# Performance work log

Measured on AMD Instinct MI355X. Metric: run time of the kernel, lower is better.

## Reference

```python
import jax, jax.numpy as jnp
import numpy as np

E = 8      # number of parts/experts
H = 128    # hidden width
D_IN = 3   # xyz coords
D_OUT = 1  # occupancy


def setup_inputs() -> dict:
    key = jax.random.key(0)
    ks = jax.random.split(key, 9)
    coords = jax.random.normal(ks[0], (1, 65536, D_IN), dtype=jnp.float32)
    s = 0.05
    return {
        "coords": coords,
        "W0": jax.random.normal(ks[1], (E, H, D_IN), dtype=jnp.float32) * s,
        "b0": jax.random.normal(ks[2], (E, H), dtype=jnp.float32) * s,
        "W1": jax.random.normal(ks[3], (E, H, H), dtype=jnp.float32) * s,
        "b1": jax.random.normal(ks[4], (E, H), dtype=jnp.float32) * s,
        "W2": jax.random.normal(ks[5], (E, H, H), dtype=jnp.float32) * s,
        "b2": jax.random.normal(ks[6], (E, H), dtype=jnp.float32) * s,
        "Wo": jax.random.normal(ks[7], (E, D_OUT, H), dtype=jnp.float32) * s,
        "bo": jax.random.normal(ks[8], (E, D_OUT), dtype=jnp.float32) * s,
    }


def reference(coords, W0, b0, W1, b1, W2, b2, Wo, bo):
    # Batched (grouped) MLP over experts: equivalent to vmap(functional_call)
    # over stacked per-part parameters in the torch module.
    # coords: [B, N, 3]; weights: [E, out, in]
    h = jax.nn.relu(jnp.einsum('bnd,ehd->ebnh', coords, W0) + b0[:, None, None, :])
    h = jax.nn.relu(jnp.einsum('ebnh,egh->ebng', h, W1) + b1[:, None, None, :])
    h = jax.nn.relu(jnp.einsum('ebnh,egh->ebng', h, W2) + b2[:, None, None, :])
    expert_out = jnp.einsum('ebnh,eoh->ebno', h, Wo) + bo[:, None, None, :]  # [E,B,N,1]
    max_occ = jnp.max(expert_out, axis=0)  # combine experts via max, [B,N,1]
    return max_occ
```

## Files before the change

### kernel.cpp

```cpp
#include <hip/hip_runtime.h>

#define NE 8
#define HD 128
#define NPTS 65536
#define TM 64

typedef __bf16 bf16x8 __attribute__((ext_vector_type(8)));
typedef float f32x4 __attribute__((ext_vector_type(4)));

__device__ __forceinline__ unsigned int f2bf(float f) {
    unsigned int u = __float_as_uint(f);
    u += 0x7FFFu + ((u >> 16) & 1u);
    return u >> 16;
}
__device__ __forceinline__ float bf2f_lo(unsigned int u) { return __uint_as_float(u << 16); }
__device__ __forceinline__ float bf2f_hi(unsigned int u) { return __uint_as_float(u & 0xFFFF0000u); }

__device__ __forceinline__ unsigned int swz(int row, int byte_in_row) {
    return (unsigned int)((row * 256 + byte_in_row) ^ ((row & 7) << 4));
}

template<int NKB, int BSTR, bool BSWZ>
__device__ __forceinline__ void gemm_gA(const unsigned short* __restrict__ Ag,
                                        const char* Bb, char* Db,
                                        const float* __restrict__ bias,
                                        int w, int lane) {
    const int lr = lane & 15;
    const int lg = lane >> 4;
    const int tc = w * 32;

    f32x4 acc[2][4];
#pragma unroll
    for (int ca = 0; ca < 2; ++ca)
#pragma unroll
        for (int nb = 0; nb < 4; ++nb)
            acc[ca][nb] = (f32x4){0.f, 0.f, 0.f, 0.f};

#pragma unroll
    for (int kb = 0; kb < NKB; ++kb) {
        bf16x8 a[2], b[4];
#pragma unroll
        for (int ca = 0; ca < 2; ++ca) {
            int c = tc + ca * 16 + lr;
            a[ca] = *(const bf16x8*)(Ag + c * (NKB * 32) + kb * 32 + lg * 8);
        }
#pragma unroll
        for (int nb = 0; nb < 4; ++nb) {
            int r = nb * 16 + lr;
            int byte = kb * 64 + lg * 16;
            const char* p = BSWZ ? (Bb + swz(r, byte)) : (Bb + r * BSTR + byte);
            b[nb] = *(const bf16x8*)p;
        }
#pragma unroll
        for (int ca = 0; ca < 2; ++ca)
#pragma unroll
            for (int nb = 0; nb < 4; ++nb)
                acc[ca][nb] = __builtin_amdgcn_mfma_f32_16x16x32_bf16(a[ca], b[nb], acc[ca][nb], 0, 0, 0);
    }

#pragma unroll
    for (int ca = 0; ca < 2; ++ca) {
        int c0 = tc + ca * 16 + lg * 4;
        float4 bs = *(const float4*)(bias + c0);
#pragma unroll
        for (int nb = 0; nb < 4; ++nb) {
            int r = nb * 16 + lr;
            f32x4 v = acc[ca][nb];
            float v0 = fmaxf(v[0] + bs.x, 0.f);
            float v1 = fmaxf(v[1] + bs.y, 0.f);
            float v2 = fmaxf(v[2] + bs.z, 0.f);
            float v3 = fmaxf(v[3] + bs.w, 0.f);
            uint2 p;
            p.x = f2bf(v0) | (f2bf(v1) << 16);
            p.y = f2bf(v2) | (f2bf(v3) << 16);
            *(uint2*)(Db + swz(r, c0 * 2)) = p;
        }
    }
}

__global__ void prep_kernel(const float* __restrict__ W0,
                            const float* __restrict__ W1,
                            const float* __restrict__ W2,
                            unsigned int* __restrict__ W1b,
                            unsigned int* __restrict__ W2b,
                            unsigned int* __restrict__ W0p) {
    int i = blockIdx.x * 256 + threadIdx.x;
    float2 v = *(const float2*)(W1 + 2 * i);
    W1b[i] = f2bf(v.x) | (f2bf(v.y) << 16);
    float2 u = *(const float2*)(W2 + 2 * i);
    W2b[i] = f2bf(u.x) | (f2bf(u.y) << 16);
    if (i < NE * HD * 16) {
        int row = i >> 4;
        int kk = (i & 15) * 2;
        float a = (kk < 3) ? W0[row * 3 + kk] : 0.f;
        float b = (kk + 1 < 3) ? W0[row * 3 + kk + 1] : 0.f;
        W0p[i] = f2bf(a) | (f2bf(b) << 16);
    }
}

__global__ __launch_bounds__(256, 4) void moe_main(
    const float* __restrict__ coords,
    const float* __restrict__ b0, const float* __restrict__ b1,
    const float* __restrict__ b2,
    const float* __restrict__ Wo, const float* __restrict__ bo,
    const unsigned short* __restrict__ W0p,
    const unsigned short* __restrict__ W1b,
    const unsigned short* __restrict__ W2b,
    float* __restrict__ out) {
    __shared__ __align__(16) unsigned short hA[TM * HD];
    __shared__ __align__(16) unsigned short hB[TM * HD];
    __shared__ __align__(16) unsigned short Xp[TM * 40];
    __shared__ __align__(16) float wos[HD];

    const int tid = threadIdx.x;
    const int lane = tid & 63;
    const int w = tid >> 6;
    const int row0 = blockIdx.x * TM;

    for (int i = tid; i < TM * 40; i += 256) Xp[i] = 0;
    __syncthreads();
    if (tid < TM * 3) {
        int r = tid / 3, k = tid % 3;
        Xp[r * 40 + k] = (unsigned short)f2bf(coords[row0 * 3 + tid]);
    }
    __syncthreads();

    float bmax = -3.0e38f;
    const int dr = tid >> 2, dq = tid & 3;

    for (int e = 0; e < NE; ++e) {
        if (tid < HD) wos[tid] = Wo[e * HD + tid];
        gemm_gA<1, 80, false>(W0p + e * HD * 32, (const char*)Xp, (char*)hA, b0 + e * HD, w, lane);
        __syncthreads();
        gemm_gA<4, 0, true>(W1b + e * HD * HD, (const char*)hA, (char*)hB, b1 + e * HD, w, lane);
        __syncthreads();
        gemm_gA<4, 0, true>(W2b + e * HD * HD, (const char*)hB, (char*)hA, b2 + e * HD, w, lane);
        __syncthreads();
        float s = 0.f;
        const char* base = (const char*)hA;
#pragma unroll
        for (int j = 0; j < 4; ++j) {
            uint4 qv = *(const uint4*)(base + swz(dr, dq * 64 + j * 16));
            int k0 = dq * 32 + j * 8;
            float4 wa = *(const float4*)(wos + k0);
            float4 wb = *(const float4*)(wos + k0 + 4);
            s += bf2f_lo(qv.x) * wa.x + bf2f_hi(qv.x) * wa.y
               + bf2f_lo(qv.y) * wa.z + bf2f_hi(qv.y) * wa.w
               + bf2f_lo(qv.z) * wb.x + bf2f_hi(qv.z) * wb.y
               + bf2f_lo(qv.w) * wb.z + bf2f_hi(qv.w) * wb.w;
        }
        s += __shfl_xor(s, 1);
        s += __shfl_xor(s, 2);
        bmax = fmaxf(bmax, s + bo[e]);
        __syncthreads();
    }
    if (dq == 0) out[row0 + dr] = bmax;
}

extern "C" void kernel_launch(void* const* d_in, const int* in_sizes, int n_in,
                              void* d_out, int out_size, void* d_ws, size_t ws_size,
                              hipStream_t stream) {
    const float* coords = (const float*)d_in[0];
    const float* W0 = (const float*)d_in[1];
    const float* b0 = (const float*)d_in[2];
    const float* W1 = (const float*)d_in[3];
    const float* b1 = (const float*)d_in[4];
    const float* W2 = (const float*)d_in[5];
    const float* b2 = (const float*)d_in[6];
    const float* Wo = (const float*)d_in[7];
    const float* bo = (const float*)d_in[8];
    float* out = (float*)d_out;

    char* ws = (char*)d_ws;
    unsigned short* W1b = (unsigned short*)(ws);
    unsigned short* W2b = (unsigned short*)(ws + 262144);
    unsigned short* W0p = (unsigned short*)(ws + 524288);

    prep_kernel<<<dim3(256), dim3(256), 0, stream>>>(
        W0, W1, W2, (unsigned int*)W1b, (unsigned int*)W2b, (unsigned int*)W0p);

    moe_main<<<dim3(NPTS / TM), dim3(256), 0, stream>>>(
        coords, b0, b1, b2, Wo, bo, W0p, W1b, W2b, out);
}
```

Measured before the change: 90.95 us.

## Prefetch weight fragments into registers and fuse output projection into layer-2 epilogue

Weight A-fragments for the next GEMM stage are loaded into registers ahead of the barrier so global loads overlap the current MFMA work. The final layer no longer writes to LDS; bias, ReLU and the Wo dot product are done in registers, reduced across lanes with shuffles, and combined across waves through a small partial-sum buffer. __syncthreads is replaced by a raw lgkmcnt wait plus s_barrier, and bf16 conversion uses the native cast. This raises register pressure under launch_bounds(256,4), and the raw barrier relies on no global stores needing to be ordered before it.

```diff
diff --git a/kernel.cpp b/kernel.cpp
--- a/kernel.cpp
+++ b/kernel.cpp
@@ -6,6 +6,7 @@
 #define TM 64
 
 typedef __bf16 bf16x8 __attribute__((ext_vector_type(8)));
+typedef __bf16 bf16x4 __attribute__((ext_vector_type(4)));
 typedef float f32x4 __attribute__((ext_vector_type(4)));
 
 __device__ __forceinline__ unsigned int f2bf(float f) {
@@ -13,37 +14,38 @@
     u += 0x7FFFu + ((u >> 16) & 1u);
     return u >> 16;
 }
-__device__ __forceinline__ float bf2f_lo(unsigned int u) { return __uint_as_float(u << 16); }
-__device__ __forceinline__ float bf2f_hi(unsigned int u) { return __uint_as_float(u & 0xFFFF0000u); }
 
 __device__ __forceinline__ unsigned int swz(int row, int byte_in_row) {
     return (unsigned int)((row * 256 + byte_in_row) ^ ((row & 7) << 4));
 }
 
-template<int NKB, int BSTR, bool BSWZ>
-__device__ __forceinline__ void gemm_gA(const unsigned short* __restrict__ Ag,
-                                        const char* Bb, char* Db,
-                                        const float* __restrict__ bias,
-                                        int w, int lane) {
-    const int lr = lane & 15;
-    const int lg = lane >> 4;
-    const int tc = w * 32;
-
-    f32x4 acc[2][4];
+__device__ __forceinline__ void bar_lds() {
+    asm volatile("s_waitcnt lgkmcnt(0)\ns_barrier" ::: "memory");
+}
+
+template<int KB0, int KB1>
+__device__ __forceinline__ void loadA128(const unsigned short* __restrict__ Ag,
+                                         bf16x8 (&a)[2][4], int tc, int lr, int lg) {
 #pragma unroll
     for (int ca = 0; ca < 2; ++ca)
 #pragma unroll
-        for (int nb = 0; nb < 4; ++nb)
-            acc[ca][nb] = (f32x4){0.f, 0.f, 0.f, 0.f};
-
+        for (int kb = KB0; kb < KB1; ++kb)
+            a[ca][kb] = *(const bf16x8*)(Ag + (tc + ca * 16 + lr) * HD + kb * 32 + lg * 8);
+}
+
+__device__ __forceinline__ void loadA32(const unsigned short* __restrict__ Ag,
+                                        bf16x8 (&a)[2][1], int tc, int lr, int lg) {
+#pragma unroll
+    for (int ca = 0; ca < 2; ++ca)
+        a[ca][0] = *(const bf16x8*)(Ag + (tc + ca * 16 + lr) * 32 + lg * 8);
+}
+
+template<int NKB, bool BSWZ, int BSTR>
+__device__ __forceinline__ void gemm_core(const bf16x8 (&a)[2][NKB], const char* Bb,
+                                          f32x4 (&acc)[2][4], int lr, int lg) {
 #pragma unroll
     for (int kb = 0; kb < NKB; ++kb) {
-        bf16x8 a[2], b[4];
-#pragma unroll
-        for (int ca = 0; ca < 2; ++ca) {
-            int c = tc + ca * 16 + lr;
-            a[ca] = *(const bf16x8*)(Ag + c * (NKB * 32) + kb * 32 + lg * 8);
-        }
+        bf16x8 b[4];
 #pragma unroll
         for (int nb = 0; nb < 4; ++nb) {
             int r = nb * 16 + lr;
@@ -55,9 +57,13 @@
         for (int ca = 0; ca < 2; ++ca)
 #pragma unroll
             for (int nb = 0; nb < 4; ++nb)
-                acc[ca][nb] = __builtin_amdgcn_mfma_f32_16x16x32_bf16(a[ca], b[nb], acc[ca][nb], 0, 0, 0);
-    }
-
+                acc[ca][nb] = __builtin_amdgcn_mfma_f32_16x16x32_bf16(a[ca][kb], b[nb], acc[ca][nb], 0, 0, 0);
+    }
+}
+
+__device__ __forceinline__ void epi_store(const f32x4 (&acc)[2][4], char* Db,
+                                          const float* __restrict__ bias,
+                                          int tc, int lr, int lg) {
 #pragma unroll
     for (int ca = 0; ca < 2; ++ca) {
         int c0 = tc + ca * 16 + lg * 4;
@@ -65,15 +71,12 @@
 #pragma unroll
         for (int nb = 0; nb < 4; ++nb) {
             int r = nb * 16 + lr;
-            f32x4 v = acc[ca][nb];
-            float v0 = fmaxf(v[0] + bs.x, 0.f);
-            float v1 = fmaxf(v[1] + bs.y, 0.f);
-            float v2 = fmaxf(v[2] + bs.z, 0.f);
-            float v3 = fmaxf(v[3] + bs.w, 0.f);
-            uint2 p;
-            p.x = f2bf(v0) | (f2bf(v1) << 16);
-            p.y = f2bf(v2) | (f2bf(v3) << 16);
-            *(uint2*)(Db + swz(r, c0 * 2)) = p;
+            bf16x4 pk;
+            pk[0] = (__bf16)fmaxf(acc[ca][nb][0] + bs.x, 0.f);
+            pk[1] = (__bf16)fmaxf(acc[ca][nb][1] + bs.y, 0.f);
+            pk[2] = (__bf16)fmaxf(acc[ca][nb][2] + bs.z, 0.f);
+            pk[3] = (__bf16)fmaxf(acc[ca][nb][3] + bs.w, 0.f);
+            *(bf16x4*)(Db + swz(r, c0 * 2)) = pk;
         }
     }
 }
@@ -109,52 +112,98 @@
     float* __restrict__ out) {
     __shared__ __align__(16) unsigned short hA[TM * HD];
     __shared__ __align__(16) unsigned short hB[TM * HD];
-    __shared__ __align__(16) unsigned short Xp[TM * 40];
-    __shared__ __align__(16) float wos[HD];
+    __shared__ __align__(16) unsigned short Xp[TM * 32];
+    __shared__ __align__(16) float part[256];
 
     const int tid = threadIdx.x;
     const int lane = tid & 63;
     const int w = tid >> 6;
+    const int lr = lane & 15;
+    const int lg = lane >> 4;
+    const int tc = w * 32;
     const int row0 = blockIdx.x * TM;
 
-    for (int i = tid; i < TM * 40; i += 256) Xp[i] = 0;
+    for (int i = tid; i < TM * 32; i += 256) Xp[i] = 0;
     __syncthreads();
     if (tid < TM * 3) {
         int r = tid / 3, k = tid % 3;
-        Xp[r * 40 + k] = (unsigned short)f2bf(coords[row0 * 3 + tid]);
+        Xp[r * 32 + k] = (unsigned short)f2bf(coords[row0 * 3 + tid]);
     }
     __syncthreads();
 
     float bmax = -3.0e38f;
-    const int dr = tid >> 2, dq = tid & 3;
+    bf16x8 a0[2][1], a1[2][4], a2[2][4];
+    loadA32(W0p, a0, tc, lr, lg);
 
     for (int e = 0; e < NE; ++e) {
-        if (tid < HD) wos[tid] = Wo[e * HD + tid];
-        gemm_gA<1, 80, false>(W0p + e * HD * 32, (const char*)Xp, (char*)hA, b0 + e * HD, w, lane);
-        __syncthreads();
-        gemm_gA<4, 0, true>(W1b + e * HD * HD, (const char*)hA, (char*)hB, b1 + e * HD, w, lane);
-        __syncthreads();
-        gemm_gA<4, 0, true>(W2b + e * HD * HD, (const char*)hB, (char*)hA, b2 + e * HD, w, lane);
-        __syncthreads();
-        float s = 0.f;
-        const char* base = (const char*)hA;
-#pragma unroll
-        for (int j = 0; j < 4; ++j) {
-            uint4 qv = *(const uint4*)(base + swz(dr, dq * 64 + j * 16));
-            int k0 = dq * 32 + j * 8;
-            float4 wa = *(const float4*)(wos + k0);
-            float4 wb = *(const float4*)(wos + k0 + 4);
-            s += bf2f_lo(qv.x) * wa.x + bf2f_hi(qv.x) * wa.y
-               + bf2f_lo(qv.y) * wa.z + bf2f_hi(qv.y) * wa.w
-               + bf2f_lo(qv.z) * wb.x + bf2f_hi(qv.z) * wb.y
-               + bf2f_lo(qv.w) * wb.z + bf2f_hi(qv.w) * wb.w;
-        }
-        s += __shfl_xor(s, 1);
-        s += __shfl_xor(s, 2);
-        bmax = fmaxf(bmax, s + bo[e]);
-        __syncthreads();
-    }
-    if (dq == 0) out[row0 + dr] = bmax;
+        const unsigned short* W1e = W1b + e * HD * HD;
+        const unsigned short* W2e = W2b + e * HD * HD;
+
+        loadA128<0, 2>(W1e, a1, tc, lr, lg);
+        f32x4 acc[2][4];
+#pragma unroll
+        for (int ca = 0; ca < 2; ++ca)
+#pragma unroll
+            for (int nb = 0; nb < 4; ++nb) acc[ca][nb] = (f32x4){0.f, 0.f, 0.f, 0.f};
+        gemm_core<1, false, 64>(a0, (const char*)Xp, acc, lr, lg);
+        epi_store(acc, (char*)hA, b0 + e * HD, tc, lr, lg);
+        bar_lds();
+
+        loadA128<2, 4>(W1e, a1, tc, lr, lg);
+        loadA128<0, 2>(W2e, a2, tc, lr, lg);
+#pragma unroll
+        for (int ca = 0; ca < 2; ++ca)
+#pragma unroll
+            for (int nb = 0; nb < 4; ++nb) acc[ca][nb] = (f32x4){0.f, 0.f, 0.f, 0.f};
+        gemm_core<4, true, 0>(a1, (const char*)hA, acc, lr, lg);
+        epi_store(acc, (char*)hB, b1 + e * HD, tc, lr, lg);
+        bar_lds();
+
+        loadA128<2, 4>(W2e, a2, tc, lr, lg);
+        loadA32(W0p + (e < 7 ? e + 1 : 7) * HD * 32, a0, tc, lr, lg);
+#pragma unroll
+        for (int ca = 0; ca < 2; ++ca)
+#pragma unroll
+            for (int nb = 0; nb < 4; ++nb) acc[ca][nb] = (f32x4){0.f, 0.f, 0.f, 0.f};
+        gemm_core<4, true, 0>(a2, (const char*)hB, acc, lr, lg);
+
+        {
+            const float* b2e = b2 + e * HD;
+            const float* Woe = Wo + e * HD;
+            float s[4] = {0.f, 0.f, 0.f, 0.f};
+#pragma unroll
+            for (int ca = 0; ca < 2; ++ca) {
+                int c0 = tc + ca * 16 + lg * 4;
+                float4 bs = *(const float4*)(b2e + c0);
+                float4 wo = *(const float4*)(Woe + c0);
+#pragma unroll
+                for (int nb = 0; nb < 4; ++nb) {
+                    float v0 = fmaxf(acc[ca][nb][0] + bs.x, 0.f);
+                    float v1 = fmaxf(acc[ca][nb][1] + bs.y, 0.f);
+                    float v2 = fmaxf(acc[ca][nb][2] + bs.z, 0.f);
+                    float v3 = fmaxf(acc[ca][nb][3] + bs.w, 0.f);
+                    s[nb] += v0 * wo.x + v1 * wo.y + v2 * wo.z + v3 * wo.w;
+                }
+            }
+#pragma unroll
+            for (int nb = 0; nb < 4; ++nb) {
+                s[nb] += __shfl_xor(s[nb], 16);
+                s[nb] += __shfl_xor(s[nb], 32);
+            }
+            if (lg == 0) {
+#pragma unroll
+                for (int nb = 0; nb < 4; ++nb) part[w * 64 + nb * 16 + lr] = s[nb];
+            }
+        }
+        bar_lds();
+
+        if (tid < TM) {
+            float v = part[tid] + part[64 + tid] + part[128 + tid] + part[192 + tid] + bo[e];
+            bmax = fmaxf(bmax, v);
+        }
+    }
+
+    if (tid < TM) out[row0 + tid] = bmax;
 }
 
 extern "C" void kernel_launch(void* const* d_in, const int* in_sizes, int n_in,
```

After: 78.35 us. 13.9% less time.
